# Performance work log

Hardware: AMD Instinct MI355X
Metric: run time of the kernel (lower is better)

Reference implementation:

```python
import jax, jax.numpy as jnp
import numpy as np

# DNC dims: N memory slots, WM word size, R read heads, H controller hidden, D word_vec
N, WM, R, H, D = 256, 64, 4, 512, 512
T, B = 128, 32
EPS = 1e-6
IFACE = R*WM + R + WM + 1 + WM + WM + R + 1 + 1 + 3*R  # DNC interface vector size


def setup_inputs() -> dict:
    key = jax.random.key(0)
    k = jax.random.split(key, 8)
    in_dim = D + R*WM  # controller sees [x_t ; flattened read vectors]
    w = lambda kk, shape: jax.random.normal(kk, shape, jnp.float32) * 0.02
    return {
        "emb_utt": jax.random.normal(k[0], (T, B, D), jnp.float32),
        "Wx": w(k[1], (in_dim, 4*H)),
        "Wh": w(k[2], (H, 4*H)),
        "b_lstm": jnp.zeros((4*H,), jnp.float32),
        "W_pre": w(k[3], (H, D)),
        "b_pre": jnp.zeros((D,), jnp.float32),
        "W_iface": w(k[4], (H, IFACE)),
        "b_iface": jnp.zeros((IFACE,), jnp.float32),
        "W_rout": w(k[5], (R*WM, D)),
    }


def _content(M, keys, beta):
    # M: (B,N,WM); keys: (B,K,WM); beta: (B,K) -> content weighting (B,K,N)
    Mn = M / jnp.maximum(jnp.linalg.norm(M, axis=-1, keepdims=True), EPS)
    kn = keys / jnp.maximum(jnp.linalg.norm(keys, axis=-1, keepdims=True), EPS)
    sim = jnp.einsum('bkw,bnw->bkn', kn, Mn)
    return jax.nn.softmax(beta[..., None] * sim, axis=-1)


def _allocation(u):
    # usage-sort-based allocation weighting (Graves et al. 2016)
    idx = jnp.argsort(u, axis=1)  # ascending usage
    su = jnp.take_along_axis(u, idx, axis=1)
    excl = jnp.concatenate([jnp.ones_like(su[:, :1]), jnp.cumprod(su, axis=1)[:, :-1]], axis=1)
    a_sorted = (1.0 - su) * excl
    bidx = jnp.arange(u.shape[0])[:, None]
    return jnp.zeros_like(u).at[bidx, idx].set(a_sorted)


def reference(emb_utt, Wx, Wh, b_lstm, W_pre, b_pre, W_iface, b_iface, W_rout):
    Bsz = emb_utt.shape[1]
    eye = jnp.eye(N, dtype=emb_utt.dtype)

    def step(carry, x):
        h, c, M, usage, rw, ww, prec, link, rvec = carry
        # ---- controller (LSTM) ----
        xin = jnp.concatenate([x, rvec.reshape(Bsz, -1)], axis=1)
        gates = xin @ Wx + h @ Wh + b_lstm
        i, f, g, o = jnp.split(gates, 4, axis=1)
        c = jax.nn.sigmoid(f) * c + jax.nn.sigmoid(i) * jnp.tanh(g)
        h = jax.nn.sigmoid(o) * jnp.tanh(c)
        # ---- interface ----
        z = h @ W_iface + b_iface
        off = [0]
        def take(n):
            v = z[:, off[0]:off[0]+n]; off[0] += n; return v
        read_keys = take(R*WM).reshape(Bsz, R, WM)
        read_str = 1.0 + jax.nn.softplus(take(R))
        write_key = take(WM)
        write_str = 1.0 + jax.nn.softplus(take(1))
        erase = jax.nn.sigmoid(take(WM))
        write_vec = take(WM)
        free = jax.nn.sigmoid(take(R))
        alloc_g = jax.nn.sigmoid(take(1))
        write_g = jax.nn.sigmoid(take(1))
        modes = jax.nn.softmax(take(3*R).reshape(Bsz, R, 3), axis=-1)
        # ---- memory write ----
        retention = jnp.prod(1.0 - free[:, :, None] * rw, axis=1)   # (B,N)
        usage = (usage + ww - usage * ww) * retention
        alloc = _allocation(usage)
        cw = _content(M, write_key[:, None, :], write_str)[:, 0, :]  # (B,N)
        ww = write_g * (alloc_g * alloc + (1.0 - alloc_g) * cw)
        M = M * (1.0 - ww[:, :, None] * erase[:, None, :]) + ww[:, :, None] * write_vec[:, None, :]
        # temporal link matrix + precedence
        link = (1.0 - ww[:, :, None] - ww[:, None, :]) * link + ww[:, :, None] * prec[:, None, :]
        link = link * (1.0 - eye)
        prec = (1.0 - jnp.sum(ww, axis=1, keepdims=True)) * prec + ww
        # ---- memory read ----
        cr = _content(M, read_keys, read_str)                        # (B,R,N)
        fw = jnp.einsum('bij,brj->bri', link, rw)                    # forward
        bw = jnp.einsum('bji,brj->bri', link, rw)                    # backward
        rw = modes[..., 0:1] * bw + modes[..., 1:2] * cr + modes[..., 2:3] * fw
        rvec = jnp.einsum('brn,bnw->brw', rw, M)
        out = h @ W_pre + b_pre + rvec.reshape(Bsz, -1) @ W_rout
        return (h, c, M, usage, rw, ww, prec, link, rvec), out

    z = lambda *s: jnp.zeros(s, jnp.float32)
    carry0 = (z(Bsz, H), z(Bsz, H), jnp.full((Bsz, N, WM), EPS, jnp.float32),
              z(Bsz, N), z(Bsz, R, N), z(Bsz, N), z(Bsz, N),
              z(Bsz, N, N), z(Bsz, R, WM))
    _, outs = jax.lax.scan(step, carry0, emb_utt)
    return outs  # (T, B, D)
```

## Files before the change

kernel.cpp:

```cpp
#include <hip/hip_runtime.h>
#include <math.h>

#define TN   256
#define TWM  64
#define TR   4
#define TH   512
#define TD   512
#define TT   128
#define TB   32
#define IFACE 471
#define EPSI 1e-6f

#define OFF_H      0
#define OFF_C      32768
#define OFF_M      49152
#define OFF_USAGE  573440
#define OFF_RW     581632
#define OFF_WW     614400
#define OFF_PRECA  622592
#define OFF_LINK   638976
#define OFF_RVEC   2736128
#define OFF_MNORM  2744320
#define OFF_ZP     2752512
#define OFF_PARSE  2998272
#define OFF_CRS    3012608
#define OFF_FW     3045376
#define OFF_BWP    3078144
#define OFF_CNT    3340288
#define TOTAL_STATE 3341696

#define CNT_ZPG(g) (OFF_CNT + (g)*16)
#define CNT_SB(b)  (OFF_CNT + (8+(b))*16)
#define CNT_FA(b)  (OFF_CNT + (40+(b))*16)
#define CNT_GG(g)  (OFF_CNT + (72+(g))*16)

__device__ __forceinline__ float sigm(float x)  { return 1.0f / (1.0f + expf(-x)); }
__device__ __forceinline__ float softpl(float x){ return x > 20.0f ? x : log1pf(expf(x)); }

__device__ __forceinline__ float ldc(const float* p) {
    return __hip_atomic_load(p, __ATOMIC_RELAXED, __HIP_MEMORY_SCOPE_AGENT);
}
__device__ __forceinline__ void stc(float* p, float v) {
    __hip_atomic_store(p, v, __ATOMIC_RELAXED, __HIP_MEMORY_SCOPE_AGENT);
}
__device__ __forceinline__ float4 ldcv4(const float* p) {
    float4 v;
    v.x = ldc(p); v.y = ldc(p + 1); v.z = ldc(p + 2); v.w = ldc(p + 3);
    return v;
}
__device__ __forceinline__ void stcv4(float* p, float4 v) {
    stc(p, v.x); stc(p + 1, v.y); stc(p + 2, v.z); stc(p + 3, v.w);
}
__device__ __forceinline__ unsigned ldcu(const unsigned* p) {
    return __hip_atomic_load(p, __ATOMIC_RELAXED, __HIP_MEMORY_SCOPE_AGENT);
}

__global__ void k_init(float* ws) {
    int idx = blockIdx.x * 256 + threadIdx.x;
    if (idx >= TOTAL_STATE) return;
    float v = 0.0f;
    if (idx >= OFF_M && idx < OFF_M + TB*TN*TWM) v = EPSI;
    if (idx >= OFF_MNORM && idx < OFF_MNORM + TB*TN) v = 8e-6f;
    ws[idx] = v;
}

__device__ __forceinline__ void out_phase(
    const float* __restrict__ W_pre, const float* __restrict__ b_pre,
    const float* __restrict__ W_rout, const float* __restrict__ ws,
    float* __restrict__ out, float* sm, const int tid, const int B2, const int t)
{
    float* act_s = sm;
    float* red_s = sm + 3072;
    const int q = B2 >> 5, s = (B2 >> 3) & 3, bg = B2 & 7, b0 = bg * 4;
    for (int i = tid; i < 768; i += 512) {
        const int bb = i / 192;
        const int k0 = (i - bb*192) * 4;
        const float* src = (k0 < 512) ? &ws[OFF_H + (t&1)*(TB*TH) + (b0+bb)*TH + k0]
                                      : &ws[OFF_RVEC + (b0+bb)*256 + (k0 - 512)];
        *(float4*)&act_s[bb*768 + k0] = *(const float4*)src;
    }
    __syncthreads();
    const int c0 = q*128 + s*32;
    const int col = tid & 31;
    const int ksb = tid >> 5;
    float a0=0, a1=0, a2=0, a3=0;
    for (int kk = ksb*48; kk < ksb*48 + 48; ++kk) {
        const float w = (kk < 512) ? W_pre[(size_t)kk * 512 + c0 + col]
                                   : W_rout[(size_t)(kk - 512) * 512 + c0 + col];
        a0 += act_s[kk]        * w;
        a1 += act_s[768 + kk]  * w;
        a2 += act_s[1536 + kk] * w;
        a3 += act_s[2304 + kk] * w;
    }
    red_s[(ksb*4 + 0)*32 + col] = a0;
    red_s[(ksb*4 + 1)*32 + col] = a1;
    red_s[(ksb*4 + 2)*32 + col] = a2;
    red_s[(ksb*4 + 3)*32 + col] = a3;
    __syncthreads();
    if (tid < 128) {
        const int cc = tid & 31, bb = tid >> 5;
        float ssum = 0.0f;
        #pragma unroll
        for (int ks2 = 0; ks2 < 16; ++ks2) ssum += red_s[(ks2*4 + bb)*32 + cc];
        ssum += b_pre[c0 + cc];
        out[(size_t)(t - 1) * (TB * TD) + (b0+bb) * TD + c0 + cc] = ssum;
    }
    __syncthreads();
}

__device__ void stepA_fn(const float* __restrict__ b_if, float* __restrict__ ws,
                         const int t, const int b, const int tid, float* sm)
{
    float* z_s      = sm + 0;
    float* rwf_s    = sm + 480;
    float* ww_old_s = sm + 1504;
    float* ww_s     = sm + 1760;
    float* u_s      = sm + 2016;
    float* prec_s   = sm + 2272;
    float* mnorm_s  = sm + 2528;
    float* alloc_s  = sm + 2784;
    float* cw_s     = sm + 3040;
    float* keysp    = sm + 3296;
    float* wkey_s   = sm + 3552;
    float* erase_s  = sm + 3616;
    float* wvec_s   = sm + 3680;
    float* rstr_s   = sm + 3744;
    float* free_s   = sm + 3748;
    float* modesp   = sm + 3752;
    float* knorm_s  = sm + 3764;
    float* sredA_s  = sm + 3772;
    float* sc_s     = sm + 3780;
    float* Pt_s     = sm + 3788;

    const float* wsM = ws + OFF_M + b * (TN * TWM);
    const float* precOld = ws + OFF_PRECA + (t & 1) * (TB * TN) + b * 256;
    float* precNew = ws + OFF_PRECA + ((t + 1) & 1) * (TB * TN) + b * 256;

    if (tid < 256)       { *(float4*)&rwf_s[tid*4] = *(const float4*)&ws[OFF_RW + b*1024 + tid*4]; }
    else if (tid < 320)  { const int i = tid-256; *(float4*)&ww_old_s[i*4] = *(const float4*)&ws[OFF_WW + b*256 + i*4]; }
    else if (tid < 384)  { const int i = tid-320; *(float4*)&u_s[i*4]      = *(const float4*)&ws[OFF_USAGE + b*256 + i*4]; }
    else if (tid < 448)  { const int i = tid-384; *(float4*)&prec_s[i*4]   = *(const float4*)&precOld[i*4]; }
    else                 { const int i = tid-448; *(float4*)&mnorm_s[i*4]  = *(const float4*)&ws[OFF_MNORM + b*256 + i*4]; }
    if (tid < IFACE) {
        float part[16];
        #pragma unroll
        for (int p = 0; p < 16; ++p)
            part[p] = ldc(&ws[OFF_ZP + ((size_t)p*32 + b) * 480 + tid]);
        float zv = b_if[tid];
        #pragma unroll
        for (int p = 0; p < 16; ++p) zv += part[p];
        z_s[tid] = zv;
    }
    __syncthreads();

    if (tid < IFACE) {
        const float v = z_s[tid];
        if (tid < 256)       keysp[(tid >> 6)*64 + (tid & 63)] = v;
        else if (tid < 260)  rstr_s[tid - 256] = 1.0f + softpl(v);
        else if (tid < 324)  wkey_s[tid - 260] = v;
        else if (tid == 324) sc_s[0] = 1.0f + softpl(v);
        else if (tid < 389)  erase_s[tid - 325] = sigm(v);
        else if (tid < 453)  wvec_s[tid - 389] = v;
        else if (tid < 457)  free_s[tid - 453] = sigm(v);
        else if (tid == 457) sc_s[1] = sigm(v);
        else if (tid == 458) sc_s[2] = sigm(v);
    }
    __syncthreads();
    if (tid < 320) {
        const int w5 = tid >> 6, lane = tid & 63;
        const float v = (w5 == 0) ? wkey_s[lane] : keysp[(w5 - 1)*64 + lane];
        float s = v * v;
        #pragma unroll
        for (int m = 1; m <= 32; m <<= 1) s += __shfl_xor(s, m);
        if (lane == 0) knorm_s[w5] = fmaxf(sqrtf(s), EPSI);
    } else if (tid >= 508) {
        const int r = tid - 508;
        const float m0 = z_s[459 + r*3], m1 = z_s[460 + r*3], m2 = z_s[461 + r*3];
        const float mx = fmaxf(m0, fmaxf(m1, m2));
        const float e0 = expf(m0 - mx), e1 = expf(m1 - mx), e2 = expf(m2 - mx);
        const float s = e0 + e1 + e2;
        modesp[r*3+0] = e0 / s; modesp[r*3+1] = e1 / s; modesp[r*3+2] = e2 / s;
    }
    __syncthreads();

    if (tid < 404) {
        float v;
        if (tid < 256)       v = keysp[tid];
        else if (tid < 320)  v = erase_s[tid - 256];
        else if (tid < 384)  v = wvec_s[tid - 320];
        else if (tid < 388)  v = rstr_s[tid - 384];
        else if (tid < 392)  v = knorm_s[tid - 388 + 1];
        else                 v = modesp[tid - 392];
        stc(&ws[OFF_PARSE + b * 448 + tid], v);
    }
    if (tid < 256) {
        float ret = 1.0f;
        #pragma unroll
        for (int r = 0; r < 4; ++r) ret *= 1.0f - free_s[r] * rwf_s[r*256 + tid];
        const float un = (u_s[tid] + ww_old_s[tid] - u_s[tid] * ww_old_s[tid]) * ret;
        u_s[tid] = un;
        ws[OFF_USAGE + b * 256 + tid] = un;
    }
    __syncthreads();

    {
        const int q = tid >> 8, n = tid & 255;
        const float un = u_s[n];
        float p = 1.0f;
        #pragma unroll 8
        for (int m = q * 128; m < q * 128 + 128; ++m) {
            const float um = u_s[m];
            const bool lt = (um < un) || (um == un && m < n);
            p *= lt ? um : 1.0f;
        }
        Pt_s[q * 256 + n] = p;
    }
    __syncthreads();
    if (tid < 256)
        alloc_s[tid] = (1.0f - u_s[tid]) * Pt_s[tid] * Pt_s[256 + tid];
    __syncthreads();

    {
        const int n = tid >> 1, q2 = tid & 1;
        const float* mp = wsM + n * 64 + q2 * 32;
        float s = 0.0f;
        #pragma unroll
        for (int it = 0; it < 8; ++it) {
            float4 mv = *(const float4*)(mp + it * 4);
            float4 kv = *(const float4*)&wkey_s[q2 * 32 + it * 4];
            s += mv.x*kv.x + mv.y*kv.y + mv.z*kv.z + mv.w*kv.w;
        }
        s += __shfl_xor(s, 1);
        if (q2 == 0) cw_s[n] = sc_s[0] * s / (knorm_s[0] * mnorm_s[n]);
    }
    __syncthreads();
    {
        float v = 0.0f, e = 0.0f;
        if (tid < 256) {
            v = cw_s[tid];
            float m = v;
            #pragma unroll
            for (int mm = 1; mm <= 32; mm <<= 1) m = fmaxf(m, __shfl_xor(m, mm));
            if ((tid & 63) == 0) sredA_s[tid >> 6] = m;
        }
        __syncthreads();
        if (tid == 0) sc_s[4] = fmaxf(fmaxf(sredA_s[0], sredA_s[1]), fmaxf(sredA_s[2], sredA_s[3]));
        __syncthreads();
        if (tid < 256) {
            e = expf(v - sc_s[4]);
            float s2 = e;
            #pragma unroll
            for (int mm = 1; mm <= 32; mm <<= 1) s2 += __shfl_xor(s2, mm);
            if ((tid & 63) == 0) sredA_s[tid >> 6] = s2;
        }
        __syncthreads();
        if (tid == 0) sc_s[5] = sredA_s[0] + sredA_s[1] + sredA_s[2] + sredA_s[3];
        __syncthreads();
        if (tid < 256) cw_s[tid] = e / sc_s[5];
    }
    __syncthreads();

    if (tid < 256) {
        const float wwn = sc_s[2] * (sc_s[1] * alloc_s[tid] + (1.0f - sc_s[1]) * cw_s[tid]);
        ww_s[tid] = wwn;
        stc(&ws[OFF_WW + b * 256 + tid], wwn);
    }
    __syncthreads();
    if (tid < 256) {
        float s = ww_s[tid];
        #pragma unroll
        for (int mm = 1; mm <= 32; mm <<= 1) s += __shfl_xor(s, mm);
        if ((tid & 63) == 0) sredA_s[tid >> 6] = s;
    }
    __syncthreads();
    if (tid == 0) sc_s[3] = sredA_s[0] + sredA_s[1] + sredA_s[2] + sredA_s[3];
    __syncthreads();
    if (tid < 256)
        precNew[tid] = (1.0f - sc_s[3]) * prec_s[tid] + ww_s[tid];
}

__device__ void stepB_fn(float* __restrict__ ws, const int t, const int b,
                         const int tid, float* sm)
{
    float* crp     = sm;
    float* rw2_s   = sm + 1024;
    float* Lt2     = sm + 2048;
    float* md      = sm + 4096;
    float* sredA_s = sm + 4112;
    float* sredB_s = sm + 4120;
    float* gmax_s  = sm + 4128;
    float* gsum_s  = sm + 4132;
    const float* wsM = ws + OFF_M + b * (TN * TWM);

    crp[tid]       = ldc(&ws[OFF_CRS + b*1024 + tid]);
    crp[tid + 512] = ldc(&ws[OFF_CRS + b*1024 + tid + 512]);
    if (tid < 12) md[tid] = ldc(&ws[OFF_PARSE + b*448 + 392 + tid]);
    __syncthreads();

    {
        const int rr = tid >> 8, n = tid & 255, wv = tid >> 6, lane = tid & 63;
        float v0 = crp[rr*256 + n], v1 = crp[(rr + 2)*256 + n];
        float m0 = v0, m1 = v1;
        #pragma unroll
        for (int mm = 1; mm <= 32; mm <<= 1) {
            m0 = fmaxf(m0, __shfl_xor(m0, mm));
            m1 = fmaxf(m1, __shfl_xor(m1, mm));
        }
        if (lane == 0) { sredA_s[wv] = m0; sredB_s[wv] = m1; }
        __syncthreads();
        if (tid < 4) {
            const float* base = (tid & 2) ? sredB_s : sredA_s;
            const int off = (tid & 1) * 4;
            gmax_s[tid] = fmaxf(fmaxf(base[off], base[off+1]), fmaxf(base[off+2], base[off+3]));
        }
        __syncthreads();
        const float e0 = expf(v0 - gmax_s[rr]);
        const float e1 = expf(v1 - gmax_s[rr + 2]);
        float s0 = e0, s1 = e1;
        #pragma unroll
        for (int mm = 1; mm <= 32; mm <<= 1) {
            s0 += __shfl_xor(s0, mm); s1 += __shfl_xor(s1, mm);
        }
        if (lane == 0) { sredA_s[wv] = s0; sredB_s[wv] = s1; }
        __syncthreads();
        if (tid < 4) {
            const float* base = (tid & 2) ? sredB_s : sredA_s;
            const int off = (tid & 1) * 4;
            gsum_s[tid] = base[off] + base[off+1] + base[off+2] + base[off+3];
        }
        __syncthreads();
        crp[rr*256 + n]       = e0 / gsum_s[rr];
        crp[(rr + 2)*256 + n] = e1 / gsum_s[rr + 2];
    }
    __syncthreads();

    {
        const int rr = tid >> 8, n = tid & 255;
        #pragma unroll
        for (int p = 0; p < 2; ++p) {
            const int r = rr + 2 * p;
            float part[8];
            #pragma unroll
            for (int c = 0; c < 8; ++c)
                part[c] = ldc(&ws[OFF_BWP + (size_t)(b*8 + c)*1024 + r*256 + n]);
            const float fwv = ldc(&ws[OFF_FW + b*1024 + r*256 + n]);
            float bw = 0.0f;
            #pragma unroll
            for (int c = 0; c < 8; ++c) bw += part[c];
            const float v = md[r*3] * bw + md[r*3+1] * crp[r*256 + n] + md[r*3+2] * fwv;
            rw2_s[r*256 + n] = v;
            ws[OFF_RW + b*1024 + r*256 + n] = v;
        }
    }
    __syncthreads();

    {
        const int g8 = tid >> 6, w = tid & 63;
        float p0=0, p1=0, p2=0, p3=0;
        const float* mb = wsM + (size_t)(g8 * 32) * 64 + w;
        for (int gg = 0; gg < 4; ++gg) {
            float mv[8];
            #pragma unroll
            for (int j = 0; j < 8; ++j) mv[j] = ldc(mb + (gg*8 + j) * 64);
            #pragma unroll
            for (int j = 0; j < 8; ++j) {
                const int n = g8*32 + gg*8 + j;
                p0 += rw2_s[n]       * mv[j];
                p1 += rw2_s[256 + n] * mv[j];
                p2 += rw2_s[512 + n] * mv[j];
                p3 += rw2_s[768 + n] * mv[j];
            }
        }
        Lt2[(g8*4 + 0)*64 + w] = p0;
        Lt2[(g8*4 + 1)*64 + w] = p1;
        Lt2[(g8*4 + 2)*64 + w] = p2;
        Lt2[(g8*4 + 3)*64 + w] = p3;
    }
    __syncthreads();
    if (tid < 256) {
        const int r = tid >> 6, w = tid & 63;
        float s = 0.0f;
        #pragma unroll
        for (int g = 0; g < 8; ++g) s += Lt2[(g*4 + r)*64 + w];
        ws[OFF_RVEC + b * 256 + tid] = s;
    }
}

__global__ __launch_bounds__(512) void k_all(
    const float* __restrict__ emb, const float* __restrict__ Wx,
    const float* __restrict__ Wh,  const float* __restrict__ b_lstm,
    const float* __restrict__ W_pre, const float* __restrict__ b_pre,
    const float* __restrict__ W_rout,
    const float* __restrict__ W_if, const float* __restrict__ b_if,
    float* __restrict__ ws, float* __restrict__ out, int t)
{
    __shared__ __align__(16) float sm[16384];
    __shared__ int myBatch;
    __shared__ int isTail;
    const int tid = threadIdx.x;
    const int blk = blockIdx.x;

    if (blk >= 128) {
        if (t > 0) {
            const int raw2 = blk - 128;
            const int B2 = (((raw2 >> 2) & 3) << 5) | ((raw2 & 3) << 3) | (raw2 >> 4);
            out_phase(W_pre, b_pre, W_rout, ws, out, sm, tid, B2, t);
        }
    } else if (t < TT) {
        const int ublk = ((blk & 7) << 4) | (blk >> 3);
        const int u0  = ublk * 4;
        {
            const int cg  = tid & 3;
            const int bg  = (tid >> 2) & 7;
            const int ks  = tid >> 5;
            const int col0 = cg * 512 + u0;
            const float* hbuf = ws + OFF_H + (t & 1) * (TB * TH);

            float acc[4][4] = {};

            for (int tile = 0; tile < 5; ++tile) {
                const int T0 = tile * 256;
                {
                    const int b = tid & 31, kf4 = tid >> 5;
                    #pragma unroll
                    for (int i = 0; i < 4; ++i) {
                        const int kf = kf4 * 4 + i;
                        const int kl = kf * 4;
                        const int k  = T0 + kl;
                        const float* src;
                        if (k < 512)      src = emb + (size_t)t * (TB*TD) + b * TD + k;
                        else if (k < 768) src = ws + OFF_RVEC + b * 256 + (k - 512);
                        else              src = hbuf + b * TH + (k - 768);
                        float4 v = *(const float4*)src;
                        sm[(kl+0)*32 + b] = v.x;
                        sm[(kl+1)*32 + b] = v.y;
                        sm[(kl+2)*32 + b] = v.z;
                        sm[(kl+3)*32 + b] = v.w;
                    }
                }
                __syncthreads();
                {
                    const int k0 = T0 + ks * 16;
                    const float* wp = (k0 < 768 ? Wx + (size_t)k0 * 2048
                                                : Wh + (size_t)(k0 - 768) * 2048) + col0;
                    const float* ap = &sm[(ks * 16) * 32 + bg * 4];
                    #pragma unroll 8
                    for (int kk = 0; kk < 16; ++kk) {
                        float4 wv = *(const float4*)wp; wp += 2048;
                        float4 av = *(const float4*)ap; ap += 32;
                        acc[0][0] += wv.x*av.x; acc[0][1] += wv.x*av.y; acc[0][2] += wv.x*av.z; acc[0][3] += wv.x*av.w;
                        acc[1][0] += wv.y*av.x; acc[1][1] += wv.y*av.y; acc[1][2] += wv.y*av.z; acc[1][3] += wv.y*av.w;
                        acc[2][0] += wv.z*av.x; acc[2][1] += wv.z*av.y; acc[2][2] += wv.z*av.z; acc[2][3] += wv.z*av.w;
                        acc[3][0] += wv.w*av.x; acc[3][1] += wv.w*av.y; acc[3][2] += wv.w*av.z; acc[3][3] += wv.w*av.w;
                    }
                }
                __syncthreads();
            }

            {
                const int rbase = 8192 + ks * 512 + (cg * 8 + bg) * 16;
                *(float4*)&sm[rbase + 0]  = make_float4(acc[0][0], acc[0][1], acc[0][2], acc[0][3]);
                *(float4*)&sm[rbase + 4]  = make_float4(acc[1][0], acc[1][1], acc[1][2], acc[1][3]);
                *(float4*)&sm[rbase + 8]  = make_float4(acc[2][0], acc[2][1], acc[2][2], acc[2][3]);
                *(float4*)&sm[rbase + 12] = make_float4(acc[3][0], acc[3][1], acc[3][2], acc[3][3]);
            }
            __syncthreads();
            {
                const int o = tid;
                float s = 0.0f;
                #pragma unroll
                for (int kq = 0; kq < 16; ++kq) s += sm[8192 + kq * 512 + o];
                const int ocg = o >> 7, obg = (o >> 4) & 7, odu = (o >> 2) & 3, obb = o & 3;
                s += b_lstm[ocg * 512 + u0 + odu];
                sm[(ocg * 4 + odu) * 32 + (obg * 4 + obb)] = s;
            }
            __syncthreads();
            if (tid < 128) {
                const int du = tid >> 5, b = tid & 31;
                const float ig = sm[(0  + du) * 32 + b];
                const float fg = sm[(4  + du) * 32 + b];
                const float gg = sm[(8  + du) * 32 + b];
                const float og = sm[(12 + du) * 32 + b];
                const int ci = b * TH + u0 + du;
                const float cold = ws[OFF_C + ci];
                const float cn = sigm(fg) * cold + sigm(ig) * tanhf(gg);
                const float hn = sigm(og) * tanhf(cn);
                ws[OFF_C + ci] = cn;
                stc(&ws[OFF_H + ((t + 1) & 1) * (TB * TH) + ci], hn);
            }
        }
        asm volatile("s_waitcnt vmcnt(0)" ::: "memory");
        __syncthreads();
        if (tid == 0)
            __hip_atomic_fetch_add((unsigned*)(ws + CNT_GG(ublk >> 3)), 1u,
                                   __ATOMIC_RELAXED, __HIP_MEMORY_SCOPE_AGENT);

        const int bgz = blk >> 4;
        const int q = (blk >> 2) & 3, s = blk & 3;
        const int b0 = bgz * 4;
        if (tid == 0) {
            const unsigned* gg = (const unsigned*)(ws + CNT_GG(q*4 + s));
            while (ldcu(gg) < 8u * (unsigned)(t + 1)) __builtin_amdgcn_s_sleep(1);
        }
        __syncthreads();
        {
            float* h1_s = sm;
            if (tid < 128) {
                const int bb = tid >> 5, kk = tid & 31;
                h1_s[bb*32 + kk] = ldc(&ws[OFF_H + ((t+1)&1)*(TB*TH) + (b0+bb)*TH + q*128 + s*32 + kk]);
            }
            __syncthreads();
            if (tid < IFACE) {
                const int col = tid;
                float a0=0, a1=0, a2=0, a3=0;
                const float* wb = W_if + (size_t)(q*128 + s*32) * IFACE + col;
                #pragma unroll 8
                for (int kk = 0; kk < 32; ++kk) {
                    const float w = *wb; wb += IFACE;
                    a0 += h1_s[kk]      * w;
                    a1 += h1_s[32+kk]   * w;
                    a2 += h1_s[64+kk]   * w;
                    a3 += h1_s[96+kk]   * w;
                }
                const size_t base = OFF_ZP + ((size_t)(q*4+s)*32 + b0) * 480 + col;
                stc(&ws[base],        a0);
                stc(&ws[base + 480],  a1);
                stc(&ws[base + 960],  a2);
                stc(&ws[base + 1440], a3);
            }
        }
        asm volatile("s_waitcnt vmcnt(0)" ::: "memory");
        __syncthreads();
        if (tid == 0) {
            unsigned* cnt = (unsigned*)(ws + CNT_ZPG(bgz));
            const unsigned old = __hip_atomic_fetch_add(cnt, 1u, __ATOMIC_RELAXED, __HIP_MEMORY_SCOPE_AGENT);
            const unsigned base = 16u * (unsigned)t;
            int mb = -1;
            if (old >= base + 12u) {
                mb = b0 + (int)(old - (base + 12u));
                while (ldcu(cnt) < base + 16u) __builtin_amdgcn_s_sleep(1);
            }
            myBatch = mb;
        }
        __syncthreads();
        if (myBatch >= 0) {
            stepA_fn(b_if, ws, t, myBatch, tid, sm);
            asm volatile("s_waitcnt vmcnt(0)" ::: "memory");
            __syncthreads();
            if (tid == 0)
                __hip_atomic_store((unsigned*)(ws + CNT_FA(myBatch)), (unsigned)(t + 1),
                                   __ATOMIC_RELAXED, __HIP_MEMORY_SCOPE_AGENT);
        }
        __syncthreads();
    }

    if (t >= TT) return;

    const int b = blk >> 3;
    const int c = blk & 7;
    {
        float* ww_s   = sm;
        float* prec_s = sm + 256;
        float* rw_s   = sm + 512;
        float* pk_s   = sm + 1536;
        float* Lt     = sm + 2048;
        const float* precOld = ws + OFF_PRECA + (t & 1) * (TB * TN) + b * 256;

        float4 m_pre;
        {
            const int ric = tid >> 4, c4 = (tid & 15) * 4;
            const int gi  = c * 32 + ric;
            m_pre = *(const float4*)(ws + OFF_M + b * (TN*TWM) + gi * 64 + c4);
        }
        float lpre[16];
        {
            const int j = tid & 255, p = tid >> 8;
            #pragma unroll
            for (int it = 0; it < 16; ++it) {
                const int ric = it * 2 + p;
                lpre[it] = ws[OFF_LINK + (size_t)b * (TN*TN) + (size_t)(c*32 + ric) * 256 + j];
            }
        }
        if (tid < 256)      { *(float4*)&rw_s[tid*4] = *(const float4*)&ws[OFF_RW + b*1024 + tid*4]; }
        else if (tid < 320) { const int i = tid-256; *(float4*)&prec_s[i*4] = *(const float4*)&precOld[i*4]; }

        if (tid == 0) {
            const unsigned* fa = (const unsigned*)(ws + CNT_FA(b));
            while (ldcu(fa) < (unsigned)(t + 1)) __builtin_amdgcn_s_sleep(1);
        }
        __syncthreads();

        if (tid < 64)                      { *(float4*)&ww_s[tid*4] = ldcv4(&ws[OFF_WW + b*256 + tid*4]); }
        else if (tid >= 384 && tid < 496)  { const int i = tid-384; *(float4*)&pk_s[i*4] = ldcv4(&ws[OFF_PARSE + b*448 + i*4]); }
        __syncthreads();

        {
            const int ric = tid >> 4, c4 = (tid & 15) * 4;
            const int gi  = c * 32 + ric;
            float* mp = ws + OFF_M + b * (TN*TWM) + gi * 64 + c4;
            float4 m = m_pre;
            const float wwi = ww_s[gi];
            float4 er = *(const float4*)&pk_s[256 + c4];
            float4 wv = *(const float4*)&pk_s[320 + c4];
            m.x = m.x * (1.0f - wwi * er.x) + wwi * wv.x;
            m.y = m.y * (1.0f - wwi * er.y) + wwi * wv.y;
            m.z = m.z * (1.0f - wwi * er.z) + wwi * wv.z;
            m.w = m.w * (1.0f - wwi * er.w) + wwi * wv.w;
            stcv4(mp, m);
            float sn = m.x*m.x + m.y*m.y + m.z*m.z + m.w*m.w;
            float d0 = m.x*pk_s[c4]     + m.y*pk_s[c4+1]     + m.z*pk_s[c4+2]     + m.w*pk_s[c4+3];
            float d1 = m.x*pk_s[64+c4]  + m.y*pk_s[64+c4+1]  + m.z*pk_s[64+c4+2]  + m.w*pk_s[64+c4+3];
            float d2 = m.x*pk_s[128+c4] + m.y*pk_s[128+c4+1] + m.z*pk_s[128+c4+2] + m.w*pk_s[128+c4+3];
            float d3 = m.x*pk_s[192+c4] + m.y*pk_s[192+c4+1] + m.z*pk_s[192+c4+2] + m.w*pk_s[192+c4+3];
            #pragma unroll
            for (int mm = 1; mm <= 8; mm <<= 1) {
                sn += __shfl_xor(sn, mm);
                d0 += __shfl_xor(d0, mm); d1 += __shfl_xor(d1, mm);
                d2 += __shfl_xor(d2, mm); d3 += __shfl_xor(d3, mm);
            }
            if ((tid & 15) == 0) {
                const float mn = fmaxf(sqrtf(sn), EPSI);
                ws[OFF_MNORM + b*256 + gi] = mn;
                const float inv = 1.0f / mn;
                stc(&ws[OFF_CRS + b*1024 + 0*256 + gi], pk_s[384+0] * d0 * inv / pk_s[388+0]);
                stc(&ws[OFF_CRS + b*1024 + 1*256 + gi], pk_s[384+1] * d1 * inv / pk_s[388+1]);
                stc(&ws[OFF_CRS + b*1024 + 2*256 + gi], pk_s[384+2] * d2 * inv / pk_s[388+2]);
                stc(&ws[OFF_CRS + b*1024 + 3*256 + gi], pk_s[384+3] * d3 * inv / pk_s[388+3]);
            }
        }

        {
            const int j = tid & 255, p = tid >> 8;
            const float wwj = ww_s[j], pj = prec_s[j];
            #pragma unroll 4
            for (int it = 0; it < 16; ++it) {
                const int ric = it * 2 + p;
                const int gi  = c * 32 + ric;
                float* lp = ws + OFF_LINK + (size_t)b * (TN*TN) + (size_t)gi * 256 + j;
                const float wwi = ww_s[gi];
                float v = (1.0f - wwi - wwj) * lpre[it] + wwi * pj;
                if (j == gi) v = 0.0f;
                *lp = v;
                Lt[ric * 257 + j] = v;
            }
        }
        __syncthreads();

        {
            const int ric = tid >> 4, g = tid & 15;
            const int gi = c * 32 + ric;
            float f0=0, f1=0, f2=0, f3=0;
            #pragma unroll 4
            for (int jj = 0; jj < 16; ++jj) {
                const int j = g * 16 + jj;
                const float v = Lt[ric * 257 + j];
                f0 += v * rw_s[j]; f1 += v * rw_s[256+j];
                f2 += v * rw_s[512+j]; f3 += v * rw_s[768+j];
            }
            #pragma unroll
            for (int mm = 1; mm <= 8; mm <<= 1) {
                f0 += __shfl_xor(f0, mm); f1 += __shfl_xor(f1, mm);
                f2 += __shfl_xor(f2, mm); f3 += __shfl_xor(f3, mm);
            }
            if (g == 0) {
                stc(&ws[OFF_FW + b*1024 + gi],       f0);
                stc(&ws[OFF_FW + b*1024 + 256 + gi], f1);
                stc(&ws[OFF_FW + b*1024 + 512 + gi], f2);
                stc(&ws[OFF_FW + b*1024 + 768 + gi], f3);
            }
        }

        {
            const int j = tid & 255, p = tid >> 8;
            float b0=0, b1=0, b2=0, b3=0;
            #pragma unroll 4
            for (int it = 0; it < 16; ++it) {
                const int ric = p * 16 + it;
                const int gi  = c * 32 + ric;
                const float v = Lt[ric * 257 + j];
                b0 += v * rw_s[gi]; b1 += v * rw_s[256+gi];
                b2 += v * rw_s[512+gi]; b3 += v * rw_s[768+gi];
            }
            __syncthreads();
            if (p == 1) { Lt[j] = b0; Lt[256+j] = b1; Lt[512+j] = b2; Lt[768+j] = b3; }
            __syncthreads();
            if (p == 0) {
                stc(&ws[OFF_BWP + (size_t)blk*1024 + j],       b0 + Lt[j]);
                stc(&ws[OFF_BWP + (size_t)blk*1024 + 256 + j], b1 + Lt[256+j]);
                stc(&ws[OFF_BWP + (size_t)blk*1024 + 512 + j], b2 + Lt[512+j]);
                stc(&ws[OFF_BWP + (size_t)blk*1024 + 768 + j], b3 + Lt[768+j]);
            }
        }
    }

    asm volatile("s_waitcnt vmcnt(0)" ::: "memory");
    __syncthreads();
    if (tid == 0) {
        unsigned* cnt = (unsigned*)(ws + CNT_SB(b));
        const unsigned old = __hip_atomic_fetch_add(cnt, 1u, __ATOMIC_RELAXED, __HIP_MEMORY_SCOPE_AGENT);
        isTail = (old == 8u * (unsigned)t + 7u) ? 1 : 0;
    }
    __syncthreads();
    if (!isTail) return;
    stepB_fn(ws, t, b, tid, sm);
}

extern "C" void kernel_launch(void* const* d_in, const int* in_sizes, int n_in,
                              void* d_out, int out_size, void* d_ws, size_t ws_size,
                              hipStream_t stream) {
    const float* emb    = (const float*)d_in[0];
    const float* Wx     = (const float*)d_in[1];
    const float* Wh     = (const float*)d_in[2];
    const float* b_lstm = (const float*)d_in[3];
    const float* W_pre  = (const float*)d_in[4];
    const float* b_pre  = (const float*)d_in[5];
    const float* W_if   = (const float*)d_in[6];
    const float* b_if   = (const float*)d_in[7];
    const float* W_rout = (const float*)d_in[8];
    float* out = (float*)d_out;
    float* ws  = (float*)d_ws;

    k_init<<<(TOTAL_STATE + 255) / 256, 256, 0, stream>>>(ws);
    for (int t = 0; t < TT; ++t) {
        k_all<<<256, 512, 0, stream>>>(emb, Wx, Wh, b_lstm, W_pre, b_pre, W_rout,
                                       W_if, b_if, ws, out, t);
    }
    k_all<<<256, 512, 0, stream>>>(emb, Wx, Wh, b_lstm, W_pre, b_pre, W_rout,
                                   W_if, b_if, ws, out, TT);
}
```

Baseline: 7.062 ms.

## Move interface matvec into dedicated per-batch blocks and drop split-K partials

The split-K interface projection is removed. It spread work across the 128 LSTM blocks, wrote partial sums to workspace, and needed per-group counters plus an election step. Instead, 32 dedicated blocks wait on one global counter for all LSTM blocks to finish, then each computes the full 512-long interface matvec for its batch inside stepA. The output projection work is remapped onto the remaining blocks, with the first 32 of them handling two tiles each. This removes one cross-block synchronisation level and the partial-sum round trip. In exchange, each stepA block now does a serial 512-step strided weight read, which may lengthen the per-step critical path.

```diff
diff --git a/kernel.cpp b/kernel.cpp
--- a/kernel.cpp
+++ b/kernel.cpp
@@ -29,10 +29,9 @@
 #define OFF_CNT    3340288
 #define TOTAL_STATE 3341696
 
-#define CNT_ZPG(g) (OFF_CNT + (g)*16)
+#define CNT_GALL   (OFF_CNT + 0*16)
 #define CNT_SB(b)  (OFF_CNT + (8+(b))*16)
 #define CNT_FA(b)  (OFF_CNT + (40+(b))*16)
-#define CNT_GG(g)  (OFF_CNT + (72+(g))*16)
 
 __device__ __forceinline__ float sigm(float x)  { return 1.0f / (1.0f + expf(-x)); }
 __device__ __forceinline__ float softpl(float x){ return x > 20.0f ? x : log1pf(expf(x)); }
@@ -53,6 +52,10 @@
 }
 __device__ __forceinline__ unsigned ldcu(const unsigned* p) {
     return __hip_atomic_load(p, __ATOMIC_RELAXED, __HIP_MEMORY_SCOPE_AGENT);
+}
+
+__device__ __forceinline__ int outswz(int raw) {
+    return (((raw >> 2) & 3) << 5) | ((raw & 3) << 3) | (raw >> 4);
 }
 
 __global__ void k_init(float* ws) {
@@ -108,7 +111,8 @@
     __syncthreads();
 }
 
-__device__ void stepA_fn(const float* __restrict__ b_if, float* __restrict__ ws,
+__device__ void stepA_fn(const float* __restrict__ W_if, const float* __restrict__ b_if,
+                         float* __restrict__ ws,
                          const int t, const int b, const int tid, float* sm)
 {
     float* z_s      = sm + 0;
@@ -131,6 +135,7 @@
     float* sredA_s  = sm + 3772;
     float* sc_s     = sm + 3780;
     float* Pt_s     = sm + 3788;
+    float* h_s      = sm + 4304;
 
     const float* wsM = ws + OFF_M + b * (TN * TWM);
     const float* precOld = ws + OFF_PRECA + (t & 1) * (TB * TN) + b * 256;
@@ -141,14 +146,15 @@
     else if (tid < 384)  { const int i = tid-320; *(float4*)&u_s[i*4]      = *(const float4*)&ws[OFF_USAGE + b*256 + i*4]; }
     else if (tid < 448)  { const int i = tid-384; *(float4*)&prec_s[i*4]   = *(const float4*)&precOld[i*4]; }
     else                 { const int i = tid-448; *(float4*)&mnorm_s[i*4]  = *(const float4*)&ws[OFF_MNORM + b*256 + i*4]; }
+    h_s[tid] = ldc(&ws[OFF_H + ((t+1)&1)*(TB*TH) + b*TH + tid]);
+    __syncthreads();
+
     if (tid < IFACE) {
-        float part[16];
-        #pragma unroll
-        for (int p = 0; p < 16; ++p)
-            part[p] = ldc(&ws[OFF_ZP + ((size_t)p*32 + b) * 480 + tid]);
         float zv = b_if[tid];
-        #pragma unroll
-        for (int p = 0; p < 16; ++p) zv += part[p];
+        const float* wb = W_if + tid;
+        #pragma unroll 8
+        for (int k = 0; k < TH; ++k)
+            zv += h_s[k] * wb[(size_t)k * IFACE];
         z_s[tid] = zv;
     }
     __syncthreads();
@@ -395,18 +401,21 @@
     float* __restrict__ ws, float* __restrict__ out, int t)
 {
     __shared__ __align__(16) float sm[16384];
-    __shared__ int myBatch;
     __shared__ int isTail;
     const int tid = threadIdx.x;
     const int blk = blockIdx.x;
 
-    if (blk >= 128) {
-        if (t > 0) {
-            const int raw2 = blk - 128;
-            const int B2 = (((raw2 >> 2) & 3) << 5) | ((raw2 & 3) << 3) | (raw2 >> 4);
-            out_phase(W_pre, b_pre, W_rout, ws, out, sm, tid, B2, t);
-        }
-    } else if (t < TT) {
+    if (t >= TT) {
+        if (blk >= 160) {
+            const int j0 = blk - 160;
+            out_phase(W_pre, b_pre, W_rout, ws, out, sm, tid, outswz(j0), t);
+            if (j0 < 32)
+                out_phase(W_pre, b_pre, W_rout, ws, out, sm, tid, outswz(96 + j0), t);
+        }
+        return;
+    }
+
+    if (blk < 128) {
         const int ublk = ((blk & 7) << 4) | (blk >> 3);
         const int u0  = ublk * 4;
         {
@@ -492,69 +501,30 @@
         asm volatile("s_waitcnt vmcnt(0)" ::: "memory");
         __syncthreads();
         if (tid == 0)
-            __hip_atomic_fetch_add((unsigned*)(ws + CNT_GG(ublk >> 3)), 1u,
+            __hip_atomic_fetch_add((unsigned*)(ws + CNT_GALL), 1u,
                                    __ATOMIC_RELAXED, __HIP_MEMORY_SCOPE_AGENT);
-
-        const int bgz = blk >> 4;
-        const int q = (blk >> 2) & 3, s = blk & 3;
-        const int b0 = bgz * 4;
+    } else if (blk < 160) {
+        const int ab = blk - 128;
         if (tid == 0) {
-            const unsigned* gg = (const unsigned*)(ws + CNT_GG(q*4 + s));
-            while (ldcu(gg) < 8u * (unsigned)(t + 1)) __builtin_amdgcn_s_sleep(1);
-        }
-        __syncthreads();
-        {
-            float* h1_s = sm;
-            if (tid < 128) {
-                const int bb = tid >> 5, kk = tid & 31;
-                h1_s[bb*32 + kk] = ldc(&ws[OFF_H + ((t+1)&1)*(TB*TH) + (b0+bb)*TH + q*128 + s*32 + kk]);
-            }
-            __syncthreads();
-            if (tid < IFACE) {
-                const int col = tid;
-                float a0=0, a1=0, a2=0, a3=0;
-                const float* wb = W_if + (size_t)(q*128 + s*32) * IFACE + col;
-                #pragma unroll 8
-                for (int kk = 0; kk < 32; ++kk) {
-                    const float w = *wb; wb += IFACE;
-                    a0 += h1_s[kk]      * w;
-                    a1 += h1_s[32+kk]   * w;
-                    a2 += h1_s[64+kk]   * w;
-                    a3 += h1_s[96+kk]   * w;
-                }
-                const size_t base = OFF_ZP + ((size_t)(q*4+s)*32 + b0) * 480 + col;
-                stc(&ws[base],        a0);
-                stc(&ws[base + 480],  a1);
-                stc(&ws[base + 960],  a2);
-                stc(&ws[base + 1440], a3);
-            }
-        }
+            const unsigned* p = (const unsigned*)(ws + CNT_GALL);
+            while (ldcu(p) < 128u * (unsigned)(t + 1)) __builtin_amdgcn_s_sleep(1);
+        }
+        __syncthreads();
+        stepA_fn(W_if, b_if, ws, t, ab, tid, sm);
         asm volatile("s_waitcnt vmcnt(0)" ::: "memory");
         __syncthreads();
-        if (tid == 0) {
-            unsigned* cnt = (unsigned*)(ws + CNT_ZPG(bgz));
-            const unsigned old = __hip_atomic_fetch_add(cnt, 1u, __ATOMIC_RELAXED, __HIP_MEMORY_SCOPE_AGENT);
-            const unsigned base = 16u * (unsigned)t;
-            int mb = -1;
-            if (old >= base + 12u) {
-                mb = b0 + (int)(old - (base + 12u));
-                while (ldcu(cnt) < base + 16u) __builtin_amdgcn_s_sleep(1);
-            }
-            myBatch = mb;
-        }
-        __syncthreads();
-        if (myBatch >= 0) {
-            stepA_fn(b_if, ws, t, myBatch, tid, sm);
-            asm volatile("s_waitcnt vmcnt(0)" ::: "memory");
-            __syncthreads();
-            if (tid == 0)
-                __hip_atomic_store((unsigned*)(ws + CNT_FA(myBatch)), (unsigned)(t + 1),
-                                   __ATOMIC_RELAXED, __HIP_MEMORY_SCOPE_AGENT);
-        }
-        __syncthreads();
-    }
-
-    if (t >= TT) return;
+        if (tid == 0)
+            __hip_atomic_store((unsigned*)(ws + CNT_FA(ab)), (unsigned)(t + 1),
+                               __ATOMIC_RELAXED, __HIP_MEMORY_SCOPE_AGENT);
+        __syncthreads();
+    } else {
+        if (t > 0) {
+            const int j0 = blk - 160;
+            out_phase(W_pre, b_pre, W_rout, ws, out, sm, tid, outswz(j0), t);
+            if (j0 < 32)
+                out_phase(W_pre, b_pre, W_rout, ws, out, sm, tid, outswz(96 + j0), t);
+        }
+    }
 
     const int b = blk >> 3;
     const int c = blk & 7;
```

New measurement: 9.786 ms. 1.39x slower.
